# Performance work log

Hardware: AMD Instinct MI355X
Metric: run time of the kernel (lower is better)

The kernel has to match this reference:

```python
import jax, jax.numpy as jnp
import numpy as np

DIM = 128
B, LQ, LK = 8, 2048, 2048


def setup_inputs() -> dict:
    key = jax.random.key(0)
    k1, k2, k3 = jax.random.split(key, 3)
    output = jax.random.normal(k1, (B, LQ, DIM), dtype=jnp.float32)
    context = jax.random.normal(k2, (B, LK, DIM), dtype=jnp.float32)
    mask = jax.random.randint(k3, (B, LQ, LK), 0, 2).astype(jnp.bool_)
    return {"output": output, "context": context, "mask": mask}


def reference(output, context, mask):
    temperature = jnp.asarray(np.power(DIM, 0.5), dtype=output.dtype)
    # scores: [B, Lq, Lk]
    attn = jnp.einsum('bqd,bkd->bqk', output, context) / temperature
    attn = jnp.where(mask, -jnp.inf, attn)
    out_attn = jax.nn.log_softmax(attn, axis=-1)
    p = jax.nn.softmax(attn, axis=-1)
    # dropout is identity in eval/reference mode
    out = jnp.einsum('bqk,bkd->bqd', p, context)
    return (out, out_attn)
```

## Files before the change

### kernel.cpp

```cpp
#include <hip/hip_runtime.h>
#include <cstdint>


#define DIMV 128
constexpr int BB = 8;
constexpr int LQ = 2048;
constexpr int LK = 2048;
constexpr float RTEMP = 0.08838834764831843f;

typedef _Float16 half8 __attribute__((ext_vector_type(8)));
typedef _Float16 half4v __attribute__((ext_vector_type(4)));
typedef float float4v __attribute__((ext_vector_type(4)));

__global__ __launch_bounds__(256) void prep_kernel(const float* __restrict__ q,
                                                   const float* __restrict__ ctx,
                                                   _Float16* __restrict__ Qf,
                                                   _Float16* __restrict__ Kf,
                                                   _Float16* __restrict__ Vf) {
    __shared__ float tile[32][132];
    const int tid  = threadIdx.x;
    const int mode = blockIdx.x >> 9;
    const int t    = blockIdx.x & 511;
    const int b    = t >> 6;
    const int r0   = (t & 63) * 32;
    const float4* s4 = (const float4*)((mode == 0 ? q : ctx) + ((size_t)b * 2048 + r0) * DIMV);
    for (int v = 0; v < 4; v++) {
        int off = tid + v * 256;
        float4 f = s4[off];
        int row = off >> 5, c4 = (off & 31) * 4;
        tile[row][c4 + 0] = f.x; tile[row][c4 + 1] = f.y;
        tile[row][c4 + 2] = f.z; tile[row][c4 + 3] = f.w;
    }
    __syncthreads();
    if (mode < 2) {
        _Float16* dst = (mode == 0 ? Qf : Kf) + (size_t)b * (2048 * DIMV);
        for (int c = 0; c < 2; c++) {
            int chunk = tid + c * 256;
            int t2 = chunk >> 8, kk = (chunk >> 6) & 3, lane = chunk & 63;
            int quad = lane >> 4, l16 = lane & 15;
            int r = t2 * 16 + l16, d0 = kk * 32 + quad * 8;
            half8 h;
            for (int e = 0; e < 8; e++) h[e] = (_Float16)tile[r][d0 + e];
            size_t tl = (size_t)(r0 >> 4) + t2;
            *(half8*)(dst + ((tl * 4 + kk) * 64 + lane) * 8) = h;
        }
    } else {
        _Float16* dst = Vf + (size_t)b * (2048 * DIMV);
        size_t i = r0 >> 5;
        for (int c = 0; c < 2; c++) {
            int chunk = tid + c * 256;
            int dt = chunk >> 6, lane = chunk & 63;
            int quad = lane >> 4, l16 = lane & 15;
            half8 h;
            for (int e = 0; e < 8; e++) h[e] = (_Float16)tile[quad * 8 + e][dt * 16 + l16];
            *(half8*)(dst + ((i * 8 + dt) * 64 + lane) * 8) = h;
        }
    }
}

__global__ __launch_bounds__(256, 2)
void attn_kernel(const unsigned char* __restrict__ mask,
                 const _Float16* __restrict__ Qf, const _Float16* __restrict__ Kf,
                 const _Float16* __restrict__ Vf,
                 float* __restrict__ out, float* __restrict__ out_attn) {
    constexpr int TQ = 16;
    constexpr int SSTR = 2052;
    __shared__ __attribute__((aligned(16))) _Float16 S[TQ * SSTR];
    __shared__ float redm[4][TQ];
    __shared__ float mfin[TQ];

    const int tid  = threadIdx.x;
    const int wave = tid >> 6;
    const int lane = tid & 63;
    const int l16  = lane & 15;
    const int quad = lane >> 4;

    const int b  = blockIdx.x & 7;
    const int q0 = (blockIdx.x >> 3) * TQ;
    const int qt = blockIdx.x >> 3;

    const _Float16* Qb = Qf + (size_t)b * (2048 * DIMV);
    const _Float16* Kb = Kf + (size_t)b * (2048 * DIMV);
    const _Float16* Vb = Vf + (size_t)b * (2048 * DIMV);

    half8 afrag[4];
    for (int kk = 0; kk < 4; kk++)
        afrag[kk] = *(const half8*)(Qb + (((size_t)qt * 4 + kk) * 64 + lane) * 8);

    float mloc[4];
    for (int r = 0; r < 4; r++) mloc[r] = -__builtin_inff();

    for (int ct = 0; ct < 32; ct++) {
        const int cT = wave * 32 + ct;
        const _Float16* kp = Kb + (size_t)cT * 4 * 64 * 8;
        float4v acc = (float4v){0.f, 0.f, 0.f, 0.f};
        for (int kk = 0; kk < 4; kk++) {
            half8 bf = *(const half8*)(kp + (kk * 64 + lane) * 8);
            acc = __builtin_amdgcn_mfma_f32_16x16x32_f16(afrag[kk], bf, acc, 0, 0, 0);
        }
        for (int r = 0; r < 4; r++) {
            float v = acc[r] * RTEMP;
            mloc[r] = fmaxf(mloc[r], v);
            S[(quad * 4 + r) * SSTR + cT * 16 + l16] = (_Float16)v;
        }
    }
    for (int r = 0; r < 4; r++) {
        float v = mloc[r];
        v = fmaxf(v, __shfl_xor(v, 1));
        v = fmaxf(v, __shfl_xor(v, 2));
        v = fmaxf(v, __shfl_xor(v, 4));
        v = fmaxf(v, __shfl_xor(v, 8));
        mloc[r] = v;
    }
    if (l16 == 0)
        for (int r = 0; r < 4; r++)
            redm[wave][quad * 4 + r] = mloc[r];
    __syncthreads();
    if (tid < TQ)
        mfin[tid] = fmaxf(fmaxf(redm[0][tid], redm[1][tid]), fmaxf(redm[2][tid], redm[3][tid]));
    __syncthreads();

    {
        const int row = tid >> 4;
        const int j   = tid & 15;
        const float m = mfin[row];
        const unsigned char* mrow = mask + ((size_t)b * LQ + q0 + row) * LK;
        _Float16* srow = S + row * SSTR;
        const float NEGINF = -__builtin_inff();
        float lsum = 0.f;
        for (int i = 0; i < 32; i++) {
            const int col = i * 64 + j * 4;
            half4v sv = *(half4v*)(srow + col);
            uint32_t mv = *(const uint32_t*)(mrow + col);
            for (int u = 0; u < 4; u++) {
                float s = (float)sv[u];
                if ((mv >> (8 * u)) & 0xffu) { s = NEGINF; sv[u] = (_Float16)NEGINF; }
                lsum += __expf(s - m);
            }
            *(half4v*)(srow + col) = sv;
        }
        lsum += __shfl_xor(lsum, 1);
        lsum += __shfl_xor(lsum, 2);
        lsum += __shfl_xor(lsum, 4);
        lsum += __shfl_xor(lsum, 8);
        const float logl = __logf(lsum);

        float* oa_row = out_attn + ((size_t)b * LQ + q0 + row) * LK;
        for (int i = 0; i < 32; i++) {
            const int col = i * 64 + j * 4;
            half4v sv = *(half4v*)(srow + col);
            half4v pv;
            float lp[4];
            for (int u = 0; u < 4; u++) {
                float s = (float)sv[u];
                float logp = s - m - logl;
                logp = fmaxf(logp, -1.0e30f);
                lp[u] = logp;
                pv[u] = (_Float16)__expf(logp);
            }
            float4 f = {lp[0], lp[1], lp[2], lp[3]};
            *(float4*)(oa_row + col) = f;
            *(half4v*)(srow + col) = pv;
        }
    }
    __syncthreads();

    float4v oacc[2];
    for (int ct = 0; ct < 2; ct++) oacc[ct] = (float4v){0.f, 0.f, 0.f, 0.f};
    for (int i = 0; i < 64; i++) {
        half8 pa = *(half8*)(S + (size_t)l16 * SSTR + i * 32 + quad * 8);
        for (int ct = 0; ct < 2; ct++) {
            const int dt = wave * 2 + ct;
            half8 bf = *(const half8*)(Vb + (((size_t)i * 8 + dt) * 64 + lane) * 8);
            oacc[ct] = __builtin_amdgcn_mfma_f32_16x16x32_f16(pa, bf, oacc[ct], 0, 0, 0);
        }
    }
    for (int ct = 0; ct < 2; ct++)
        for (int r = 0; r < 4; r++)
            out[((size_t)b * LQ + q0 + quad * 4 + r) * DIMV + wave * 32 + ct * 16 + l16] = oacc[ct][r];
}

extern "C" void kernel_launch(void* const* d_in, const int* in_sizes, int n_in,
                              void* d_out, int out_size, void* d_ws, size_t ws_size,
                              hipStream_t stream) {
    const float* q_f32 = (const float*)d_in[0];
    const float* c_f32 = (const float*)d_in[1];
    const unsigned char* mask = (const unsigned char*)d_in[2];

    float* out      = (float*)d_out;
    float* out_attn = out + (size_t)BB * LQ * DIMV;

    _Float16* Qf = (_Float16*)d_ws;
    _Float16* Kf = Qf + (size_t)BB * LQ * DIMV;
    _Float16* Vf = Kf + (size_t)BB * LK * DIMV;

    prep_kernel<<<1536, 256, 0, stream>>>(q_f32, c_f32, Qf, Kf, Vf);
    attn_kernel<<<BB * (LQ / 16), 256, 0, stream>>>(mask, Qf, Kf, Vf, out, out_attn);
}
```

Baseline: 287.1 us.

## Replace shared-memory score buffer with online softmax and split-K waves

The attention kernel no longer stores the full 16x2048 fp16 score row block in LDS. Each wave now processes a quarter of the keys with an online (flash-style) softmax that rescales lazily, feeds P directly from registers into 16x16x16 MFMAs against a re-laid-out V, and merges the per-wave partial results through a small LDS reduction. A second pass recomputes QK^T to write log-probabilities, and occupancy is raised to 4 blocks per CU. This trades extra QK^T compute and repeated K and mask reads for much less LDS use and removes the LDS round trips over the score buffer.

```diff
diff --git a/kernel.cpp b/kernel.cpp
--- a/kernel.cpp
+++ b/kernel.cpp
@@ -46,28 +46,33 @@
         }
     } else {
         _Float16* dst = Vf + (size_t)b * (2048 * DIMV);
-        size_t i = r0 >> 5;
+        const int kt0 = r0 >> 4;
         for (int c = 0; c < 2; c++) {
             int chunk = tid + c * 256;
-            int dt = chunk >> 6, lane = chunk & 63;
-            int quad = lane >> 4, l16 = lane & 15;
+            int ktl = chunk >> 8, dp = (chunk >> 6) & 3, ln = chunk & 63;
+            int qd = ln >> 4, s16 = ln & 15;
             half8 h;
-            for (int e = 0; e < 8; e++) h[e] = (_Float16)tile[quad * 8 + e][dt * 16 + l16];
-            *(half8*)(dst + ((i * 8 + dt) * 64 + lane) * 8) = h;
+            for (int e = 0; e < 4; e++) {
+                h[e]     = (_Float16)tile[ktl * 16 + qd * 4 + e][(2 * dp) * 16 + s16];
+                h[e + 4] = (_Float16)tile[ktl * 16 + qd * 4 + e][(2 * dp + 1) * 16 + s16];
+            }
+            *(half8*)(dst + ((((size_t)(kt0 + ktl)) * 4 + dp) * 64 + ln) * 8) = h;
         }
     }
 }
 
-__global__ __launch_bounds__(256, 2)
+__global__ __launch_bounds__(256, 4)
 void attn_kernel(const unsigned char* __restrict__ mask,
                  const _Float16* __restrict__ Qf, const _Float16* __restrict__ Kf,
                  const _Float16* __restrict__ Vf,
                  float* __restrict__ out, float* __restrict__ out_attn) {
     constexpr int TQ = 16;
-    constexpr int SSTR = 2052;
-    __shared__ __attribute__((aligned(16))) _Float16 S[TQ * SSTR];
+    __shared__ __attribute__((aligned(16))) float pvred[4][TQ][132];
     __shared__ float redm[4][TQ];
-    __shared__ float mfin[TQ];
+    __shared__ float redl[4][TQ];
+    __shared__ float swf[4][TQ];
+    __shared__ float mcl[TQ];
+    __shared__ float rls[TQ];
 
     const int tid  = threadIdx.x;
     const int wave = tid >> 6;
@@ -76,108 +81,150 @@
     const int quad = lane >> 4;
 
     const int b  = blockIdx.x & 7;
-    const int q0 = (blockIdx.x >> 3) * TQ;
     const int qt = blockIdx.x >> 3;
+    const int q0 = qt * TQ;
 
     const _Float16* Qb = Qf + (size_t)b * (2048 * DIMV);
     const _Float16* Kb = Kf + (size_t)b * (2048 * DIMV);
     const _Float16* Vb = Vf + (size_t)b * (2048 * DIMV);
 
-    half8 afrag[4];
+    half8 qfrag[4];
+#pragma unroll
     for (int kk = 0; kk < 4; kk++)
-        afrag[kk] = *(const half8*)(Qb + (((size_t)qt * 4 + kk) * 64 + lane) * 8);
-
-    float mloc[4];
-    for (int r = 0; r < 4; r++) mloc[r] = -__builtin_inff();
+        qfrag[kk] = *(const half8*)(Qb + (((size_t)qt * 4 + kk) * 64 + lane) * 8);
+
+    const unsigned char* mrow = mask + ((size_t)b * LQ + q0 + l16) * LK + wave * 512 + quad * 4;
+
+    const _Float16* kbase = Kb + (size_t)wave * 32 * 2048;
+    const _Float16* vbase = Vb + (size_t)wave * 32 * 2048;
+
+    const float NEGINF = -__builtin_inff();
+    float m = -1e30f;
+    float l = 0.f;
+    float4v oacc[8];
+#pragma unroll
+    for (int dt = 0; dt < 8; dt++) oacc[dt] = (float4v){0.f, 0.f, 0.f, 0.f};
 
     for (int ct = 0; ct < 32; ct++) {
-        const int cT = wave * 32 + ct;
-        const _Float16* kp = Kb + (size_t)cT * 4 * 64 * 8;
-        float4v acc = (float4v){0.f, 0.f, 0.f, 0.f};
+        const _Float16* kp = kbase + (size_t)ct * 2048;
+        float4v st = (float4v){0.f, 0.f, 0.f, 0.f};
+#pragma unroll
         for (int kk = 0; kk < 4; kk++) {
-            half8 bf = *(const half8*)(kp + (kk * 64 + lane) * 8);
-            acc = __builtin_amdgcn_mfma_f32_16x16x32_f16(afrag[kk], bf, acc, 0, 0, 0);
-        }
+            half8 kf = *(const half8*)(kp + (kk * 64 + lane) * 8);
+            st = __builtin_amdgcn_mfma_f32_16x16x32_f16(kf, qfrag[kk], st, 0, 0, 0);
+        }
+        const uint32_t mv = *(const uint32_t*)(mrow + ct * 16);
+        float sv[4];
+#pragma unroll
         for (int r = 0; r < 4; r++) {
-            float v = acc[r] * RTEMP;
-            mloc[r] = fmaxf(mloc[r], v);
-            S[(quad * 4 + r) * SSTR + cT * 16 + l16] = (_Float16)v;
-        }
-    }
+            float v = st[r] * RTEMP;
+            if ((mv >> (8 * r)) & 0xffu) v = NEGINF;
+            sv[r] = v;
+        }
+        float tmax = fmaxf(fmaxf(sv[0], sv[1]), fmaxf(sv[2], sv[3]));
+        tmax = fmaxf(tmax, __shfl_xor(tmax, 16));
+        tmax = fmaxf(tmax, __shfl_xor(tmax, 32));
+        const bool upd = tmax > m + 3.0f;
+        if (__any(upd)) {
+            const float mnew = upd ? tmax : m;
+            const float sc = __expf(m - mnew);
+            float scr[4];
+#pragma unroll
+            for (int r = 0; r < 4; r++) scr[r] = __shfl(sc, quad * 4 + r);
+            l *= sc;
+#pragma unroll
+            for (int dt = 0; dt < 8; dt++)
+#pragma unroll
+                for (int r = 0; r < 4; r++) oacc[dt][r] *= scr[r];
+            m = mnew;
+        }
+        half4v pa;
+        float psum = 0.f;
+#pragma unroll
+        for (int r = 0; r < 4; r++) {
+            const float p = __expf(sv[r] - m);
+            psum += p;
+            pa[r] = (_Float16)p;
+        }
+        psum += __shfl_xor(psum, 16);
+        psum += __shfl_xor(psum, 32);
+        l += psum;
+        const _Float16* vp = vbase + (size_t)ct * 2048;
+#pragma unroll
+        for (int dp = 0; dp < 4; dp++) {
+            half8 v8 = *(const half8*)(vp + (dp * 64 + lane) * 8);
+            half4v vlo = __builtin_shufflevector(v8, v8, 0, 1, 2, 3);
+            half4v vhi = __builtin_shufflevector(v8, v8, 4, 5, 6, 7);
+            oacc[2 * dp]     = __builtin_amdgcn_mfma_f32_16x16x16f16(pa, vlo, oacc[2 * dp],     0, 0, 0);
+            oacc[2 * dp + 1] = __builtin_amdgcn_mfma_f32_16x16x16f16(pa, vhi, oacc[2 * dp + 1], 0, 0, 0);
+        }
+    }
+
+    if (quad == 0) { redm[wave][l16] = m; redl[wave][l16] = l; }
+    __syncthreads();
+    if (tid < TQ) {
+        const float m0 = redm[0][tid], m1 = redm[1][tid], m2 = redm[2][tid], m3 = redm[3][tid];
+        const float M = fmaxf(fmaxf(m0, m1), fmaxf(m2, m3));
+        const float e0 = __expf(m0 - M), e1 = __expf(m1 - M);
+        const float e2 = __expf(m2 - M), e3 = __expf(m3 - M);
+        const float L = e0 * redl[0][tid] + e1 * redl[1][tid]
+                      + e2 * redl[2][tid] + e3 * redl[3][tid];
+        swf[0][tid] = e0; swf[1][tid] = e1; swf[2][tid] = e2; swf[3][tid] = e3;
+        mcl[tid] = M + __logf(L);
+        rls[tid] = 1.0f / L;
+    }
+    __syncthreads();
+
+#pragma unroll
     for (int r = 0; r < 4; r++) {
-        float v = mloc[r];
-        v = fmaxf(v, __shfl_xor(v, 1));
-        v = fmaxf(v, __shfl_xor(v, 2));
-        v = fmaxf(v, __shfl_xor(v, 4));
-        v = fmaxf(v, __shfl_xor(v, 8));
-        mloc[r] = v;
-    }
-    if (l16 == 0)
-        for (int r = 0; r < 4; r++)
-            redm[wave][quad * 4 + r] = mloc[r];
-    __syncthreads();
-    if (tid < TQ)
-        mfin[tid] = fmaxf(fmaxf(redm[0][tid], redm[1][tid]), fmaxf(redm[2][tid], redm[3][tid]));
+        const float sc = swf[wave][quad * 4 + r];
+#pragma unroll
+        for (int dt = 0; dt < 8; dt++)
+            pvred[wave][quad * 4 + r][dt * 16 + l16] = oacc[dt][r] * sc;
+    }
+
+    const float mc = mcl[l16];
+    float* oa = out_attn + ((size_t)b * LQ + q0 + l16) * LK + wave * 512 + quad * 4;
+#pragma unroll 2
+    for (int ct = 0; ct < 32; ct++) {
+        const _Float16* kp = kbase + (size_t)ct * 2048;
+        float4v st = (float4v){0.f, 0.f, 0.f, 0.f};
+#pragma unroll
+        for (int kk = 0; kk < 4; kk++) {
+            half8 kf = *(const half8*)(kp + (kk * 64 + lane) * 8);
+            st = __builtin_amdgcn_mfma_f32_16x16x32_f16(kf, qfrag[kk], st, 0, 0, 0);
+        }
+        const uint32_t mv = *(const uint32_t*)(mrow + ct * 16);
+        float4v o;
+#pragma unroll
+        for (int r = 0; r < 4; r++) {
+            float logp = st[r] * RTEMP - mc;
+            if ((mv >> (8 * r)) & 0xffu) logp = -1.0e30f;
+            o[r] = fmaxf(logp, -1.0e30f);
+        }
+        *(float4v*)(oa + ct * 16) = o;
+    }
     __syncthreads();
 
     {
         const int row = tid >> 4;
-        const int j   = tid & 15;
-        const float m = mfin[row];
-        const unsigned char* mrow = mask + ((size_t)b * LQ + q0 + row) * LK;
-        _Float16* srow = S + row * SSTR;
-        const float NEGINF = -__builtin_inff();
-        float lsum = 0.f;
-        for (int i = 0; i < 32; i++) {
-            const int col = i * 64 + j * 4;
-            half4v sv = *(half4v*)(srow + col);
-            uint32_t mv = *(const uint32_t*)(mrow + col);
-            for (int u = 0; u < 4; u++) {
-                float s = (float)sv[u];
-                if ((mv >> (8 * u)) & 0xffu) { s = NEGINF; sv[u] = (_Float16)NEGINF; }
-                lsum += __expf(s - m);
-            }
-            *(half4v*)(srow + col) = sv;
-        }
-        lsum += __shfl_xor(lsum, 1);
-        lsum += __shfl_xor(lsum, 2);
-        lsum += __shfl_xor(lsum, 4);
-        lsum += __shfl_xor(lsum, 8);
-        const float logl = __logf(lsum);
-
-        float* oa_row = out_attn + ((size_t)b * LQ + q0 + row) * LK;
-        for (int i = 0; i < 32; i++) {
-            const int col = i * 64 + j * 4;
-            half4v sv = *(half4v*)(srow + col);
-            half4v pv;
-            float lp[4];
-            for (int u = 0; u < 4; u++) {
-                float s = (float)sv[u];
-                float logp = s - m - logl;
-                logp = fmaxf(logp, -1.0e30f);
-                lp[u] = logp;
-                pv[u] = (_Float16)__expf(logp);
-            }
-            float4 f = {lp[0], lp[1], lp[2], lp[3]};
-            *(float4*)(oa_row + col) = f;
-            *(half4v*)(srow + col) = pv;
-        }
-    }
-    __syncthreads();
-
-    float4v oacc[2];
-    for (int ct = 0; ct < 2; ct++) oacc[ct] = (float4v){0.f, 0.f, 0.f, 0.f};
-    for (int i = 0; i < 64; i++) {
-        half8 pa = *(half8*)(S + (size_t)l16 * SSTR + i * 32 + quad * 8);
-        for (int ct = 0; ct < 2; ct++) {
-            const int dt = wave * 2 + ct;
-            half8 bf = *(const half8*)(Vb + (((size_t)i * 8 + dt) * 64 + lane) * 8);
-            oacc[ct] = __builtin_amdgcn_mfma_f32_16x16x32_f16(pa, bf, oacc[ct], 0, 0, 0);
-        }
-    }
-    for (int ct = 0; ct < 2; ct++)
-        for (int r = 0; r < 4; r++)
-            out[((size_t)b * LQ + q0 + quad * 4 + r) * DIMV + wave * 32 + ct * 16 + l16] = oacc[ct][r];
+        const int c0 = (tid & 15) * 8;
+        const float rcl = rls[row];
+        float* op = out + ((size_t)b * LQ + q0 + row) * DIMV + c0;
+#pragma unroll
+        for (int h = 0; h < 2; h++) {
+            const int c = c0 + h * 4;
+            float4v a0 = *(const float4v*)&pvred[0][row][c];
+            float4v a1 = *(const float4v*)&pvred[1][row][c];
+            float4v a2 = *(const float4v*)&pvred[2][row][c];
+            float4v a3 = *(const float4v*)&pvred[3][row][c];
+            float4v v;
+#pragma unroll
+            for (int j = 0; j < 4; j++)
+                v[j] = (a0[j] + a1[j] + a2[j] + a3[j]) * rcl;
+            *(float4v*)(op + h * 4) = v;
+        }
+    }
 }
 
 extern "C" void kernel_launch(void* const* d_in, const int* in_sizes, int n_in,
```

New measurement: 298.1 us. 1.04x slower.
